# Kernel optimization log

Measured on AMD Instinct MI355X. Metric: run time of the kernel, lower is better.

Reference implementation:

```python
import jax, jax.numpy as jnp
import numpy as np

N = 100000          # nodes
E = 1600000         # edges (avg degree 16)
IN_DIM = 64
HID = 64
OUT = 32
NUM_GRAPHS = 64


def setup_inputs() -> dict:
    key = jax.random.key(0)
    ks = jax.random.split(key, 12)
    x = jax.random.normal(ks[0], (N, IN_DIM), dtype=jnp.float32)
    edge_index = jax.random.randint(ks[1], (2, E), 0, N, dtype=jnp.int64)
    batch = jnp.sort(jax.random.randint(ks[2], (N,), 0, NUM_GRAPHS, dtype=jnp.int64))
    s = 0.05
    return {
        "x": x,
        "edge_index": edge_index,
        "batch": batch,
        "w1_init": jax.random.normal(ks[3], (IN_DIM, HID), dtype=jnp.float32) * s,
        "w1_root": jax.random.normal(ks[4], (IN_DIM, HID), dtype=jnp.float32) * s,
        "b1": jnp.zeros((HID,), dtype=jnp.float32),
        "w2_init": jax.random.normal(ks[5], (HID, HID), dtype=jnp.float32) * s,
        "w2_root": jax.random.normal(ks[6], (HID, HID), dtype=jnp.float32) * s,
        "b2": jnp.zeros((HID,), dtype=jnp.float32),
        "fc_w": jax.random.normal(ks[7], (HID, OUT), dtype=jnp.float32) * s,
        "fc_b": jnp.zeros((OUT,), dtype=jnp.float32),
    }


def reference(x, edge_index, batch, w1_init, w1_root, b1, w2_init, w2_root, b2, fc_w, fc_b):
    row, col = edge_index[0], edge_index[1]
    # gcn_norm without self loops (ARMAConv default): deg over target nodes
    ones_e = jnp.ones((E,), dtype=x.dtype)
    deg = jax.ops.segment_sum(ones_e, col, num_segments=N)
    dinv = jnp.where(deg > 0, jax.lax.rsqrt(jnp.maximum(deg, 1.0)), 0.0)
    norm = dinv[row] * dinv[col]  # [E]

    def propagate(h):  # out[col] += norm * h[row]
        return jax.ops.segment_sum(h[row] * norm[:, None], col, num_segments=N)

    # ARMAConv (K=1, T=1, act=None): A_hat (x W_init) + x W_root + b
    h = jax.nn.relu(propagate(x @ w1_init) + x @ w1_root + b1)
    h = jax.nn.relu(propagate(h @ w2_init) + h @ w2_root + b2)

    # global mean pool over graphs
    cnt = jax.ops.segment_sum(jnp.ones((N,), dtype=h.dtype), batch, num_segments=NUM_GRAPHS)
    pooled = jax.ops.segment_sum(h, batch, num_segments=NUM_GRAPHS) / jnp.maximum(cnt, 1.0)[:, None]

    return pooled @ fc_w + fc_b  # [NUM_GRAPHS, OUT]
```

## Files before the change

kernel.cpp:

```cpp
#include <hip/hip_runtime.h>
#include <hip/hip_bf16.h>


#define NB 256
#define CAP 5120
#define MAXB 400
#define P1_CHUNK 2048

typedef unsigned int uint32;
typedef unsigned short ushort16;
typedef __attribute__((ext_vector_type(8))) short short8;
typedef __attribute__((ext_vector_type(4))) float f32x4;

__device__ inline uint32 bf16rn(float f) {
    uint32 u = __float_as_uint(f);
    uint32 r = ((u >> 16) & 1u) + 0x7FFFu;
    return (u + r) >> 16;
}
__device__ inline uint32 pack_bf16(float a, float b) {
    return bf16rn(a) | (bf16rn(b) << 16);
}
__device__ inline float bflo(uint32 u) { return __uint_as_float(u << 16); }
__device__ inline float bfhi(uint32 u) { return __uint_as_float(u & 0xFFFF0000u); }

__global__ __launch_bounds__(256) void bucket_kernel(
    const int* __restrict__ row, const int* __restrict__ col,
    uint32* __restrict__ bpack, int* __restrict__ bcnt, int E,
    const float* __restrict__ W1i, const float* __restrict__ W1r,
    const float* __restrict__ W2i, const float* __restrict__ W2r,
    ushort16* __restrict__ wt) {
    __shared__ int hist[MAXB];
    __shared__ int ofs[MAXB];
    __shared__ int cur[MAXB];
    __shared__ int gbase[MAXB];
    __shared__ int s[256];
    __shared__ uint32 stage[P1_CHUNK];
    __shared__ unsigned short stage_bk[P1_CHUNK];

    int t = threadIdx.x;

    if (blockIdx.x < 128) {
        int idx = blockIdx.x * 256 + t;
        int m = idx >> 12;
        int r = idx & 4095;
        int d = r >> 6, k = r & 63;
        const float* W = (m < 2) ? W1i : (m < 4) ? W1r : (m < 6) ? W2i : W2r;
        float v = W[k * 64 + d];
        uint32 hi = bf16rn(v);
        uint32 outv;
        if (m & 1) {
            float hf = __uint_as_float(hi << 16);
            outv = bf16rn(v - hf);
        } else {
            outv = hi;
        }
        wt[(size_t)m * 4096 + d * 64 + k] = (unsigned short)outv;
        return;
    }

    for (int i = t; i < MAXB; i += 256) hist[i] = 0;
    __syncthreads();

    int e0 = (blockIdx.x - 128) * P1_CHUNK;
    int cntE = min(E - e0, P1_CHUNK);

    for (int i = t; i < cntE; i += 256) {
        int c = col[e0 + i];
        atomicAdd(&hist[c >> 8], 1);
    }
    __syncthreads();

    int i2 = 2 * t;
    int a = (i2 < MAXB) ? hist[i2] : 0;
    int b = (i2 + 1 < MAXB) ? hist[i2 + 1] : 0;
    s[t] = a + b;
    __syncthreads();
    for (int off = 1; off < 256; off <<= 1) {
        int x = (t >= off) ? s[t - off] : 0;
        __syncthreads();
        s[t] += x;
        __syncthreads();
    }
    int excl = (t > 0) ? s[t - 1] : 0;
    if (i2 < MAXB) ofs[i2] = excl;
    if (i2 + 1 < MAXB) ofs[i2 + 1] = excl + a;
    __syncthreads();

    for (int i = t; i < MAXB; i += 256) {
        cur[i] = ofs[i];
        gbase[i] = hist[i] ? atomicAdd(&bcnt[i], hist[i]) : 0;
    }
    __syncthreads();

    for (int i = t; i < cntE; i += 256) {
        int c = col[e0 + i];
        int r = row[e0 + i];
        int bk = c >> 8;
        int k = atomicAdd(&cur[bk], 1);
        stage[k] = ((uint32)(c & 255) << 24) | (uint32)r;
        stage_bk[k] = (unsigned short)bk;
    }
    __syncthreads();

    for (int i = t; i < cntE; i += 256) {
        uint32 pk = stage[i];
        int bk = stage_bk[i];
        int gd = gbase[bk] + (i - ofs[bk]);
        if (gd < CAP) bpack[(size_t)bk * CAP + gd] = pk;
    }
}

__global__ __launch_bounds__(1024) void csr_kernel(
    const uint32* __restrict__ bpack, const int* __restrict__ bcnt,
    int* __restrict__ es, int* __restrict__ nstart, int* __restrict__ ndeg,
    float* __restrict__ dinv, int n) {
    __shared__ uint32 sbp[CAP];
    __shared__ int h[NB];
    __shared__ int s[NB];
    __shared__ int cur[NB];
    int b = blockIdx.x, t = threadIdx.x;
    if (t < NB) h[t] = 0;
    __syncthreads();
    int cnt = min(bcnt[b], CAP);
    size_t base = (size_t)b * CAP;
    for (int i = t; i < cnt; i += 1024) {
        uint32 pk = bpack[base + i];
        sbp[i] = pk;
        atomicAdd(&h[pk >> 24], 1);
    }
    __syncthreads();
    if (t < NB) s[t] = h[t];
    __syncthreads();
    for (int off = 1; off < NB; off <<= 1) {
        int x = 0;
        if (t < NB && t >= off) x = s[t - off];
        __syncthreads();
        if (t < NB) s[t] += x;
        __syncthreads();
    }
    if (t < NB) {
        int myofs = s[t] - h[t];
        cur[t] = myofs;
        int node = b * NB + t;
        if (node < n) {
            nstart[node] = (int)base + myofs;
            ndeg[node] = h[t];
            dinv[node] = h[t] ? rsqrtf((float)h[t]) : 0.0f;
        }
    }
    __syncthreads();
    for (int i = t; i < cnt; i += 1024) {
        uint32 pk = sbp[i];
        int cl = (int)(pk >> 24);
        int p = atomicAdd(&cur[cl], 1);
        es[base + p] = (int)(pk & 0xFFFFFFu);
    }
}

__global__ __launch_bounds__(256) void gemm_mfma(
    const void* __restrict__ Xin,
    const ushort16* __restrict__ wt4,
    const float* __restrict__ bias, const float* __restrict__ dinv,
    ushort16* __restrict__ Ts, ushort16* __restrict__ Rs, int n, int xf32) {
    __shared__ unsigned short sXs[64 * 72];
    int t = threadIdx.x;
    int node0 = blockIdx.x * 64;

    if (xf32) {
        const float* X = (const float*)Xin;
        for (int i = t; i < 1024; i += 256) {
            int r = i >> 4, c4 = (i & 15) * 4;
            int node = node0 + r;
            float4 v = make_float4(0.f, 0.f, 0.f, 0.f);
            if (node < n) v = *(const float4*)&X[(size_t)node * 64 + c4];
            *(uint32*)&sXs[r * 72 + c4] = pack_bf16(v.x, v.y);
            *(uint32*)&sXs[r * 72 + c4 + 2] = pack_bf16(v.z, v.w);
        }
    } else {
        const uint32* Xb2 = (const uint32*)Xin;
        for (int i = t; i < 512; i += 256) {
            int r = i >> 3, kg = i & 7;
            int node = node0 + r;
            uint4 v = make_uint4(0u, 0u, 0u, 0u);
            if (node < n) v = *(const uint4*)&Xb2[(size_t)node * 32 + kg * 4];
            *(uint4*)&sXs[r * 72 + kg * 8] = v;
        }
    }

    int w = t >> 6;
    int lane = t & 63;
    int q = lane >> 4;
    int col = lane & 15;
    int dim = w * 16 + col;

    short8 bih[2], bil[2], brh[2], brl[2];
#pragma unroll
    for (int kh = 0; kh < 2; ++kh) {
        size_t o = (size_t)dim * 64 + kh * 32 + q * 8;
        bih[kh] = *(const short8*)&wt4[0 * 4096 + o];
        bil[kh] = *(const short8*)&wt4[1 * 4096 + o];
        brh[kh] = *(const short8*)&wt4[2 * 4096 + o];
        brl[kh] = *(const short8*)&wt4[3 * 4096 + o];
    }
    float4 bias4 = *(const float4*)&bias[w * 16 + q * 4];
    __syncthreads();

    unsigned short* TsU = (unsigned short*)Ts;
    unsigned short* RsU = (unsigned short*)Rs;

#pragma unroll
    for (int mt = 0; mt < 4; ++mt) {
        int rbase = mt * 16 + col;
        short8 a0 = *(const short8*)&sXs[rbase * 72 + q * 8];
        short8 a1 = *(const short8*)&sXs[rbase * 72 + 32 + q * 8];
        f32x4 accT = {0.f, 0.f, 0.f, 0.f};
        f32x4 accR = {0.f, 0.f, 0.f, 0.f};
        accT = __builtin_amdgcn_mfma_f32_16x16x32_bf16(bih[0], a0, accT, 0, 0, 0);
        accT = __builtin_amdgcn_mfma_f32_16x16x32_bf16(bih[1], a1, accT, 0, 0, 0);
        accT = __builtin_amdgcn_mfma_f32_16x16x32_bf16(bil[0], a0, accT, 0, 0, 0);
        accT = __builtin_amdgcn_mfma_f32_16x16x32_bf16(bil[1], a1, accT, 0, 0, 0);
        accR = __builtin_amdgcn_mfma_f32_16x16x32_bf16(brh[0], a0, accR, 0, 0, 0);
        accR = __builtin_amdgcn_mfma_f32_16x16x32_bf16(brh[1], a1, accR, 0, 0, 0);
        accR = __builtin_amdgcn_mfma_f32_16x16x32_bf16(brl[0], a0, accR, 0, 0, 0);
        accR = __builtin_amdgcn_mfma_f32_16x16x32_bf16(brl[1], a1, accR, 0, 0, 0);

        int node = node0 + mt * 16 + col;
        if (node < n) {
            float dv = dinv[node];
            uint2 pT, pR;
            pT.x = pack_bf16(accT[0] * dv, accT[1] * dv);
            pT.y = pack_bf16(accT[2] * dv, accT[3] * dv);
            pR.x = pack_bf16(accR[0] + bias4.x, accR[1] + bias4.y);
            pR.y = pack_bf16(accR[2] + bias4.z, accR[3] + bias4.w);
            size_t o = (size_t)node * 64 + w * 16 + q * 4;
            *(uint2*)&TsU[o] = pT;
            *(uint2*)&RsU[o] = pR;
        }
    }
}

__global__ __launch_bounds__(256) void gather_fused(
    const uint2* __restrict__ Ts2, const uint2* __restrict__ Rs2,
    const int* __restrict__ es, const int* __restrict__ nstart,
    const int* __restrict__ ndeg, const float* __restrict__ dinv,
    uint2* __restrict__ Hb2, int n) {
    int c = blockIdx.x * 4 + (threadIdx.x >> 6);
    if (c >= n) return;
    int lane = threadIdx.x & 63;
    int q = lane >> 4;
    int d4 = lane & 15;
    int deg = ndeg[c];
    int s0 = nstart[c];
    float a0 = 0.f, a1 = 0.f, a2 = 0.f, a3 = 0.f;
    for (int base = 0; base < deg; base += 64) {
        int m = min(deg - base, 64);
        int sid = (lane < m) ? es[s0 + base + lane] : 0;
        for (int j = 0; j < m; j += 16) {
            int e0 = j + q, e1 = j + 4 + q, e2 = j + 8 + q, e3 = j + 12 + q;
            int r0 = __shfl(sid, e0);
            int r1 = __shfl(sid, e1);
            int r2 = __shfl(sid, e2);
            int r3 = __shfl(sid, e3);
            uint2 z = make_uint2(0u, 0u);
            uint2 v0 = (e0 < m) ? Ts2[(size_t)r0 * 16 + d4] : z;
            uint2 v1 = (e1 < m) ? Ts2[(size_t)r1 * 16 + d4] : z;
            uint2 v2 = (e2 < m) ? Ts2[(size_t)r2 * 16 + d4] : z;
            uint2 v3 = (e3 < m) ? Ts2[(size_t)r3 * 16 + d4] : z;
            a0 += bflo(v0.x) + bflo(v1.x) + bflo(v2.x) + bflo(v3.x);
            a1 += bfhi(v0.x) + bfhi(v1.x) + bfhi(v2.x) + bfhi(v3.x);
            a2 += bflo(v0.y) + bflo(v1.y) + bflo(v2.y) + bflo(v3.y);
            a3 += bfhi(v0.y) + bfhi(v1.y) + bfhi(v2.y) + bfhi(v3.y);
        }
    }
    a0 += __shfl_xor(a0, 16); a0 += __shfl_xor(a0, 32);
    a1 += __shfl_xor(a1, 16); a1 += __shfl_xor(a1, 32);
    a2 += __shfl_xor(a2, 16); a2 += __shfl_xor(a2, 32);
    a3 += __shfl_xor(a3, 16); a3 += __shfl_xor(a3, 32);
    if (lane < 16) {
        float dc = dinv[c];
        uint2 ur = Rs2[(size_t)c * 16 + d4];
        float h0 = fmaxf(fmaf(dc, a0, bflo(ur.x)), 0.0f);
        float h1 = fmaxf(fmaf(dc, a1, bfhi(ur.x)), 0.0f);
        float h2 = fmaxf(fmaf(dc, a2, bflo(ur.y)), 0.0f);
        float h3 = fmaxf(fmaf(dc, a3, bfhi(ur.y)), 0.0f);
        Hb2[(size_t)c * 16 + d4] = make_uint2(pack_bf16(h0, h1), pack_bf16(h2, h3));
    }
}

__global__ __launch_bounds__(256) void pool_kernel(
    const uint32* __restrict__ Hb, const int* __restrict__ batch,
    float* __restrict__ pooled, float* __restrict__ cnt, int n) {
    __shared__ float sAcc[64 * 64];
    __shared__ float sCnt[64];
    int tid = threadIdx.x;
    for (int i = tid; i < 4096; i += 256) sAcc[i] = 0.0f;
    if (tid < 64) sCnt[tid] = 0.0f;
    __syncthreads();

    int w = tid >> 6, lane = tid & 63;
    int half = lane >> 5, d2 = lane & 31;
    int s = blockIdx.x * 64 + w * 16;
    int e = min(s + 16, n);
    float a0 = 0.0f, a1 = 0.0f, c = 0.0f;
    int gcur = -1;
    for (int i = s + half; i < e; i += 2) {
        int g = batch[i];
        if (g != gcur) {
            if (gcur >= 0) {
                atomicAdd(&sAcc[gcur * 64 + 2 * d2], a0);
                atomicAdd(&sAcc[gcur * 64 + 2 * d2 + 1], a1);
                if (d2 == 0) atomicAdd(&sCnt[gcur], c);
            }
            gcur = g; a0 = 0.0f; a1 = 0.0f; c = 0.0f;
        }
        uint32 u = Hb[(size_t)i * 32 + d2];
        a0 += bflo(u);
        a1 += bfhi(u);
        c += 1.0f;
    }
    if (gcur >= 0) {
        atomicAdd(&sAcc[gcur * 64 + 2 * d2], a0);
        atomicAdd(&sAcc[gcur * 64 + 2 * d2 + 1], a1);
        if (d2 == 0) atomicAdd(&sCnt[gcur], c);
    }
    __syncthreads();
    for (int i = tid; i < 4096; i += 256) {
        float v = sAcc[i];
        if (v != 0.0f) atomicAdd(&pooled[i], v);
    }
    if (tid < 64) {
        float v = sCnt[tid];
        if (v != 0.0f) atomicAdd(&cnt[tid], v);
    }
}

__global__ void final_fc(const float* __restrict__ pooled, const float* __restrict__ cnt,
                         const float* __restrict__ fcw, const float* __restrict__ fcb,
                         float* __restrict__ out) {
    int idx = blockIdx.x * 256 + threadIdx.x;
    if (idx >= 64 * 32) return;
    int g = idx >> 5, o = idx & 31;
    float c = fmaxf(cnt[g], 1.0f);
    float acc = 0.0f;
#pragma unroll
    for (int k = 0; k < 64; ++k) acc = fmaf(pooled[g * 64 + k], fcw[k * 32 + o], acc);
    out[idx] = acc / c + fcb[o];
}

extern "C" void kernel_launch(void* const* d_in, const int* in_sizes, int n_in,
                              void* d_out, int out_size, void* d_ws, size_t ws_size,
                              hipStream_t stream) {
    const float* x       = (const float*)d_in[0];
    const int*   eidx    = (const int*)d_in[1];
    const int*   batch   = (const int*)d_in[2];
    const float* w1_init = (const float*)d_in[3];
    const float* w1_root = (const float*)d_in[4];
    const float* b1      = (const float*)d_in[5];
    const float* w2_init = (const float*)d_in[6];
    const float* w2_root = (const float*)d_in[7];
    const float* b2      = (const float*)d_in[8];
    const float* fc_w    = (const float*)d_in[9];
    const float* fc_b    = (const float*)d_in[10];
    float* out = (float*)d_out;

    const int N = in_sizes[0] / 64;
    const int E = in_sizes[1] / 2;
    const int* row = eidx;
    const int* col = eidx + E;

    const int B = (N + NB - 1) / NB;

    uint32* bpack = (uint32*)d_ws;
    int*   es     = (int*)(bpack + (size_t)B * CAP);
    int*   bcnt   = es + (size_t)B * CAP;
    float* pooled = (float*)(bcnt + MAXB);
    float* cnt    = pooled + 64 * 64;
    int*   nstart = (int*)(cnt + 64);
    int*   ndeg   = nstart + N;
    float* dinv   = (float*)(ndeg + N);
    uint32* wtU   = (uint32*)(dinv + N);
    uint32* Ts    = wtU + 16384;
    uint32* Rs    = Ts + (size_t)N * 32;
    uint32* Hb    = Rs + (size_t)N * 32;
    ushort16* wt  = (ushort16*)wtU;

    hipMemsetAsync(bcnt, 0, (size_t)(MAXB + 64 * 64 + 64) * sizeof(int), stream);

    const int EB = (E + P1_CHUNK - 1) / P1_CHUNK;
    bucket_kernel<<<128 + EB, 256, 0, stream>>>(row, col, bpack, bcnt, E,
                                                w1_init, w1_root, w2_init, w2_root, wt);
    csr_kernel<<<B, 1024, 0, stream>>>(bpack, bcnt, es, nstart, ndeg, dinv, N);

    gemm_mfma<<<(N + 63) / 64, 256, 0, stream>>>(x, wt, b1, dinv,
                                                 (ushort16*)Ts, (ushort16*)Rs, N, 1);
    gather_fused<<<(N + 3) / 4, 256, 0, stream>>>((const uint2*)Ts, (const uint2*)Rs,
                                                  es, nstart, ndeg, dinv, (uint2*)Hb, N);

    gemm_mfma<<<(N + 63) / 64, 256, 0, stream>>>(Hb, wt + (size_t)4 * 4096, b2, dinv,
                                                 (ushort16*)Ts, (ushort16*)Rs, N, 0);
    gather_fused<<<(N + 3) / 4, 256, 0, stream>>>((const uint2*)Ts, (const uint2*)Rs,
                                                  es, nstart, ndeg, dinv, (uint2*)Hb, N);

    pool_kernel<<<(N + 63) / 64, 256, 0, stream>>>(Hb, batch, pooled, cnt, N);
    final_fc<<<(64 * 32 + 255) / 256, 256, 0, stream>>>(pooled, cnt, fc_w, fc_b, out);
}
```

Before: 288.0 us.

## Fuse first GEMM into CSR build and second GEMM into layer-1 gather

The layer-1 feature GEMM now runs inside the CSR construction kernel, reusing its shared memory and computing dinv from the local degree histogram. The layer-1 gather/aggregation now feeds its ReLU output straight into a shared-memory tile that the layer-2 GEMM consumes in the same kernel. Together these remove two launches and the global round trip of the hidden activations. The cost is 36KB of shared memory in the 1024-thread CSR block, and a gather kernel where each wave walks 16 nodes serially, which may cut latency hiding for the irregular loads.

```diff
diff --git a/kernel.cpp b/kernel.cpp
--- a/kernel.cpp
+++ b/kernel.cpp
@@ -110,14 +110,20 @@
     }
 }
 
-__global__ __launch_bounds__(1024) void csr_kernel(
+__global__ __launch_bounds__(1024) void csr_gemm(
     const uint32* __restrict__ bpack, const int* __restrict__ bcnt,
     int* __restrict__ es, int* __restrict__ nstart, int* __restrict__ ndeg,
-    float* __restrict__ dinv, int n) {
-    __shared__ uint32 sbp[CAP];
+    float* __restrict__ dinv,
+    const float* __restrict__ X, const ushort16* __restrict__ wt4,
+    const float* __restrict__ bias,
+    ushort16* __restrict__ Ts, ushort16* __restrict__ Rs, int n) {
     __shared__ int h[NB];
-    __shared__ int s[NB];
-    __shared__ int cur[NB];
+    __shared__ alignas(16) unsigned char uni[36864];
+    uint32* sbp = (uint32*)uni;
+    int* s      = (int*)(uni + 20480);
+    int* cur    = (int*)(uni + 21504);
+    unsigned short* sXs = (unsigned short*)uni;
+
     int b = blockIdx.x, t = threadIdx.x;
     if (t < NB) h[t] = 0;
     __syncthreads();
@@ -155,43 +161,23 @@
         int p = atomicAdd(&cur[cl], 1);
         es[base + p] = (int)(pk & 0xFFFFFFu);
     }
-}
-
-__global__ __launch_bounds__(256) void gemm_mfma(
-    const void* __restrict__ Xin,
-    const ushort16* __restrict__ wt4,
-    const float* __restrict__ bias, const float* __restrict__ dinv,
-    ushort16* __restrict__ Ts, ushort16* __restrict__ Rs, int n, int xf32) {
-    __shared__ unsigned short sXs[64 * 72];
-    int t = threadIdx.x;
-    int node0 = blockIdx.x * 64;
-
-    if (xf32) {
-        const float* X = (const float*)Xin;
-        for (int i = t; i < 1024; i += 256) {
-            int r = i >> 4, c4 = (i & 15) * 4;
-            int node = node0 + r;
-            float4 v = make_float4(0.f, 0.f, 0.f, 0.f);
-            if (node < n) v = *(const float4*)&X[(size_t)node * 64 + c4];
-            *(uint32*)&sXs[r * 72 + c4] = pack_bf16(v.x, v.y);
-            *(uint32*)&sXs[r * 72 + c4 + 2] = pack_bf16(v.z, v.w);
-        }
-    } else {
-        const uint32* Xb2 = (const uint32*)Xin;
-        for (int i = t; i < 512; i += 256) {
-            int r = i >> 3, kg = i & 7;
-            int node = node0 + r;
-            uint4 v = make_uint4(0u, 0u, 0u, 0u);
-            if (node < n) v = *(const uint4*)&Xb2[(size_t)node * 32 + kg * 4];
-            *(uint4*)&sXs[r * 72 + kg * 8] = v;
-        }
-    }
-
-    int w = t >> 6;
-    int lane = t & 63;
-    int q = lane >> 4;
-    int col = lane & 15;
-    int dim = w * 16 + col;
+    __syncthreads();
+
+    for (int i = t; i < 4096; i += 1024) {
+        int tile = i >> 10, j = i & 1023;
+        int r = j >> 4, c4 = (j & 15) * 4;
+        int node = b * NB + tile * 64 + r;
+        float4 v = make_float4(0.f, 0.f, 0.f, 0.f);
+        if (node < n) v = *(const float4*)&X[(size_t)node * 64 + c4];
+        *(uint32*)&sXs[tile * 4608 + r * 72 + c4] = pack_bf16(v.x, v.y);
+        *(uint32*)&sXs[tile * 4608 + r * 72 + c4 + 2] = pack_bf16(v.z, v.w);
+    }
+    __syncthreads();
+
+    int wv = t >> 6, lane = t & 63;
+    int tile = wv >> 2, wq = wv & 3;
+    int q = lane >> 4, colx = lane & 15;
+    int dim = wq * 16 + colx;
 
     short8 bih[2], bil[2], brh[2], brl[2];
 #pragma unroll
@@ -202,17 +188,16 @@
         brh[kh] = *(const short8*)&wt4[2 * 4096 + o];
         brl[kh] = *(const short8*)&wt4[3 * 4096 + o];
     }
-    float4 bias4 = *(const float4*)&bias[w * 16 + q * 4];
-    __syncthreads();
+    float4 bias4 = *(const float4*)&bias[wq * 16 + q * 4];
 
     unsigned short* TsU = (unsigned short*)Ts;
     unsigned short* RsU = (unsigned short*)Rs;
 
 #pragma unroll
     for (int mt = 0; mt < 4; ++mt) {
-        int rbase = mt * 16 + col;
-        short8 a0 = *(const short8*)&sXs[rbase * 72 + q * 8];
-        short8 a1 = *(const short8*)&sXs[rbase * 72 + 32 + q * 8];
+        int rbase = mt * 16 + colx;
+        short8 a0 = *(const short8*)&sXs[tile * 4608 + rbase * 72 + q * 8];
+        short8 a1 = *(const short8*)&sXs[tile * 4608 + rbase * 72 + 32 + q * 8];
         f32x4 accT = {0.f, 0.f, 0.f, 0.f};
         f32x4 accR = {0.f, 0.f, 0.f, 0.f};
         accT = __builtin_amdgcn_mfma_f32_16x16x32_bf16(bih[0], a0, accT, 0, 0, 0);
@@ -224,7 +209,117 @@
         accR = __builtin_amdgcn_mfma_f32_16x16x32_bf16(brl[0], a0, accR, 0, 0, 0);
         accR = __builtin_amdgcn_mfma_f32_16x16x32_bf16(brl[1], a1, accR, 0, 0, 0);
 
-        int node = node0 + mt * 16 + col;
+        int li = tile * 64 + mt * 16 + colx;
+        int node = b * NB + li;
+        if (node < n) {
+            int dg = h[li];
+            float dv = dg ? rsqrtf((float)dg) : 0.0f;
+            uint2 pT, pR;
+            pT.x = pack_bf16(accT[0] * dv, accT[1] * dv);
+            pT.y = pack_bf16(accT[2] * dv, accT[3] * dv);
+            pR.x = pack_bf16(accR[0] + bias4.x, accR[1] + bias4.y);
+            pR.y = pack_bf16(accR[2] + bias4.z, accR[3] + bias4.w);
+            size_t o = (size_t)node * 64 + wq * 16 + q * 4;
+            *(uint2*)&TsU[o] = pT;
+            *(uint2*)&RsU[o] = pR;
+        }
+    }
+}
+
+__global__ __launch_bounds__(256) void gather_gemm(
+    const uint2* __restrict__ Ts2, const uint2* __restrict__ Rs2,
+    const int* __restrict__ es, const int* __restrict__ nstart,
+    const int* __restrict__ ndeg, const float* __restrict__ dinv,
+    const ushort16* __restrict__ wt4, const float* __restrict__ bias,
+    ushort16* __restrict__ To, ushort16* __restrict__ Ro, int n) {
+    __shared__ unsigned short sHs[64 * 72];
+    int t = threadIdx.x;
+    int w = t >> 6, lane = t & 63;
+    int q = lane >> 4, d4 = lane & 15;
+    int node0 = blockIdx.x * 64;
+
+    for (int rd = 0; rd < 16; ++rd) {
+        int cl = w * 16 + rd;
+        int c = node0 + cl;
+        if (c < n) {
+            int deg = ndeg[c];
+            int s0 = nstart[c];
+            float a0 = 0.f, a1 = 0.f, a2 = 0.f, a3 = 0.f;
+            for (int base = 0; base < deg; base += 64) {
+                int m = min(deg - base, 64);
+                int sid = (lane < m) ? es[s0 + base + lane] : 0;
+                for (int j = 0; j < m; j += 16) {
+                    int e0 = j + q, e1 = j + 4 + q, e2 = j + 8 + q, e3 = j + 12 + q;
+                    int r0 = __shfl(sid, e0);
+                    int r1 = __shfl(sid, e1);
+                    int r2 = __shfl(sid, e2);
+                    int r3 = __shfl(sid, e3);
+                    uint2 z = make_uint2(0u, 0u);
+                    uint2 v0 = (e0 < m) ? Ts2[(size_t)r0 * 16 + d4] : z;
+                    uint2 v1 = (e1 < m) ? Ts2[(size_t)r1 * 16 + d4] : z;
+                    uint2 v2 = (e2 < m) ? Ts2[(size_t)r2 * 16 + d4] : z;
+                    uint2 v3 = (e3 < m) ? Ts2[(size_t)r3 * 16 + d4] : z;
+                    a0 += bflo(v0.x) + bflo(v1.x) + bflo(v2.x) + bflo(v3.x);
+                    a1 += bfhi(v0.x) + bfhi(v1.x) + bfhi(v2.x) + bfhi(v3.x);
+                    a2 += bflo(v0.y) + bflo(v1.y) + bflo(v2.y) + bflo(v3.y);
+                    a3 += bfhi(v0.y) + bfhi(v1.y) + bfhi(v2.y) + bfhi(v3.y);
+                }
+            }
+            a0 += __shfl_xor(a0, 16); a0 += __shfl_xor(a0, 32);
+            a1 += __shfl_xor(a1, 16); a1 += __shfl_xor(a1, 32);
+            a2 += __shfl_xor(a2, 16); a2 += __shfl_xor(a2, 32);
+            a3 += __shfl_xor(a3, 16); a3 += __shfl_xor(a3, 32);
+            if (lane < 16) {
+                float dc = dinv[c];
+                uint2 ur = Rs2[(size_t)c * 16 + d4];
+                float h0 = fmaxf(fmaf(dc, a0, bflo(ur.x)), 0.0f);
+                float h1 = fmaxf(fmaf(dc, a1, bfhi(ur.x)), 0.0f);
+                float h2 = fmaxf(fmaf(dc, a2, bflo(ur.y)), 0.0f);
+                float h3 = fmaxf(fmaf(dc, a3, bfhi(ur.y)), 0.0f);
+                *(uint2*)&sHs[cl * 72 + d4 * 4] =
+                    make_uint2(pack_bf16(h0, h1), pack_bf16(h2, h3));
+            }
+        } else {
+            if (lane < 16)
+                *(uint2*)&sHs[cl * 72 + d4 * 4] = make_uint2(0u, 0u);
+        }
+    }
+    __syncthreads();
+
+    int colx = lane & 15;
+    int dim = w * 16 + colx;
+
+    short8 bih[2], bil[2], brh[2], brl[2];
+#pragma unroll
+    for (int kh = 0; kh < 2; ++kh) {
+        size_t o = (size_t)dim * 64 + kh * 32 + q * 8;
+        bih[kh] = *(const short8*)&wt4[0 * 4096 + o];
+        bil[kh] = *(const short8*)&wt4[1 * 4096 + o];
+        brh[kh] = *(const short8*)&wt4[2 * 4096 + o];
+        brl[kh] = *(const short8*)&wt4[3 * 4096 + o];
+    }
+    float4 bias4 = *(const float4*)&bias[w * 16 + q * 4];
+
+    unsigned short* ToU = (unsigned short*)To;
+    unsigned short* RoU = (unsigned short*)Ro;
+
+#pragma unroll
+    for (int mt = 0; mt < 4; ++mt) {
+        int rbase = mt * 16 + colx;
+        short8 a0 = *(const short8*)&sHs[rbase * 72 + q * 8];
+        short8 a1 = *(const short8*)&sHs[rbase * 72 + 32 + q * 8];
+        f32x4 accT = {0.f, 0.f, 0.f, 0.f};
+        f32x4 accR = {0.f, 0.f, 0.f, 0.f};
+        accT = __builtin_amdgcn_mfma_f32_16x16x32_bf16(bih[0], a0, accT, 0, 0, 0);
+        accT = __builtin_amdgcn_mfma_f32_16x16x32_bf16(bih[1], a1, accT, 0, 0, 0);
+        accT = __builtin_amdgcn_mfma_f32_16x16x32_bf16(bil[0], a0, accT, 0, 0, 0);
+        accT = __builtin_amdgcn_mfma_f32_16x16x32_bf16(bil[1], a1, accT, 0, 0, 0);
+        accR = __builtin_amdgcn_mfma_f32_16x16x32_bf16(brh[0], a0, accR, 0, 0, 0);
+        accR = __builtin_amdgcn_mfma_f32_16x16x32_bf16(brh[1], a1, accR, 0, 0, 0);
+        accR = __builtin_amdgcn_mfma_f32_16x16x32_bf16(brl[0], a0, accR, 0, 0, 0);
+        accR = __builtin_amdgcn_mfma_f32_16x16x32_bf16(brl[1], a1, accR, 0, 0, 0);
+
+        int node = node0 + mt * 16 + colx;
         if (node < n) {
             float dv = dinv[node];
             uint2 pT, pR;
@@ -233,8 +328,8 @@
             pR.x = pack_bf16(accR[0] + bias4.x, accR[1] + bias4.y);
             pR.y = pack_bf16(accR[2] + bias4.z, accR[3] + bias4.w);
             size_t o = (size_t)node * 64 + w * 16 + q * 4;
-            *(uint2*)&TsU[o] = pT;
-            *(uint2*)&RsU[o] = pR;
+            *(uint2*)&ToU[o] = pT;
+            *(uint2*)&RoU[o] = pR;
         }
     }
 }
@@ -379,9 +474,10 @@
     int*   ndeg   = nstart + N;
     float* dinv   = (float*)(ndeg + N);
     uint32* wtU   = (uint32*)(dinv + N);
-    uint32* Ts    = wtU + 16384;
-    uint32* Rs    = Ts + (size_t)N * 32;
-    uint32* Hb    = Rs + (size_t)N * 32;
+    uint32* Ts1   = wtU + 16384;
+    uint32* Rs1   = Ts1 + (size_t)N * 32;
+    uint32* T2    = Rs1 + (size_t)N * 32;
+    uint32* R2    = T2 + (size_t)N * 32;
     ushort16* wt  = (ushort16*)wtU;
 
     hipMemsetAsync(bcnt, 0, (size_t)(MAXB + 64 * 64 + 64) * sizeof(int), stream);
@@ -389,18 +485,18 @@
     const int EB = (E + P1_CHUNK - 1) / P1_CHUNK;
     bucket_kernel<<<128 + EB, 256, 0, stream>>>(row, col, bpack, bcnt, E,
                                                 w1_init, w1_root, w2_init, w2_root, wt);
-    csr_kernel<<<B, 1024, 0, stream>>>(bpack, bcnt, es, nstart, ndeg, dinv, N);
-
-    gemm_mfma<<<(N + 63) / 64, 256, 0, stream>>>(x, wt, b1, dinv,
-                                                 (ushort16*)Ts, (ushort16*)Rs, N, 1);
-    gather_fused<<<(N + 3) / 4, 256, 0, stream>>>((const uint2*)Ts, (const uint2*)Rs,
-                                                  es, nstart, ndeg, dinv, (uint2*)Hb, N);
-
-    gemm_mfma<<<(N + 63) / 64, 256, 0, stream>>>(Hb, wt + (size_t)4 * 4096, b2, dinv,
-                                                 (ushort16*)Ts, (ushort16*)Rs, N, 0);
-    gather_fused<<<(N + 3) / 4, 256, 0, stream>>>((const uint2*)Ts, (const uint2*)Rs,
-                                                  es, nstart, ndeg, dinv, (uint2*)Hb, N);
-
-    pool_kernel<<<(N + 63) / 64, 256, 0, stream>>>(Hb, batch, pooled, cnt, N);
+
+    csr_gemm<<<B, 1024, 0, stream>>>(bpack, bcnt, es, nstart, ndeg, dinv,
+                                     x, wt, b1, (ushort16*)Ts1, (ushort16*)Rs1, N);
+
+    gather_gemm<<<(N + 63) / 64, 256, 0, stream>>>(
+        (const uint2*)Ts1, (const uint2*)Rs1, es, nstart, ndeg, dinv,
+        wt + (size_t)4 * 4096, b2, (ushort16*)T2, (ushort16*)R2, N);
+
+    gather_fused<<<(N + 3) / 4, 256, 0, stream>>>(
+        (const uint2*)T2, (const uint2*)R2, es, nstart, ndeg, dinv,
+        (uint2*)Ts1, N);
+
+    pool_kernel<<<(N + 63) / 64, 256, 0, stream>>>(Ts1, batch, pooled, cnt, N);
     final_fc<<<(64 * 32 + 255) / 256, 256, 0, stream>>>(pooled, cnt, fc_w, fc_b, out);
 }
```

New measurement: 282.0 us. 1.02x faster.
